# Performance work log

Measured on AMD Instinct MI355X. Metric: run time of the kernel, lower is better.

The kernel has to match this reference:

```python
import jax, jax.numpy as jnp
import numpy as np

B, N = 2, 6
FC, FH, FW = 256, 32, 88            # encoder feature shape
ORFH, ORFW = 256, 704               # original image H, W
OUT_C = 128
D_ST, D_END, D_STEP = 1.0, 60.0, 3.0
NXV, NYV, NZV = 256, 256, 1         # BEV voxel grid (x, y, z)
DXV = np.array([0.4, 0.4, 20.0], np.float32)          # dx
BXV = np.array([-51.0, -51.0, 0.0], np.float32)       # bx = bound_lo + dx/2
BN_EPS = 1e-3


def _conv(x, w, b):
    y = jax.lax.conv_general_dilated(x, w, (1, 1), 'SAME',
                                     dimension_numbers=('NCHW', 'OIHW', 'NCHW'))
    return y + b[None, :, None, None]


def _bn(x, scale, bias, mean, var):
    inv = scale / jnp.sqrt(var + BN_EPS)
    return x * inv[None, :, None, None] + (bias - mean * inv)[None, :, None, None]


def _frustum():
    ds = jnp.arange(D_ST, D_END, D_STEP, dtype=jnp.float32)      # (D,)
    xs = jnp.linspace(0.0, ORFW - 1.0, FW)
    ys = jnp.linspace(0.0, ORFH - 1.0, FH)
    f = jnp.stack(jnp.broadcast_arrays(xs[None, None, :], ys[None, :, None],
                                       ds[:, None, None]), axis=-1)  # (D,FH,FW,3)
    return f, ds


def _forward(cam2ego_rot, cam2ego_trans, cam_intrins, post_cam2ego_rot,
             post_cam2ego_trans, img_feats,
             conv1_w, conv1_b, bn1_s, bn1_b, bn1_m, bn1_v,
             conv2_w, conv2_b, bn2_s, bn2_b, bn2_m, bn2_v,
             conv3_w, conv3_b):
    frustum, depth_vals = _frustum()
    D = depth_vals.shape[0]
    # ---- geometry (GaussianLSS.get_geometry) ----
    pts = frustum[None, None] - post_cam2ego_trans[:, :, None, None, None, :]
    inv_post = jnp.linalg.inv(post_cam2ego_rot)                       # (B,N,3,3)
    pts = jnp.einsum('bnij,bndhwj->bndhwi', inv_post, pts)
    pts = jnp.concatenate([pts[..., :2] * pts[..., 2:3], pts[..., 2:3]], -1)
    combine = cam2ego_rot @ jnp.linalg.inv(cam_intrins)
    geometry = (jnp.einsum('bnij,bndhwj->bndhwi', combine, pts)
                + cam2ego_trans[:, :, None, None, None, :])           # (B,N,D,H,W,3)
    # ---- depth net + gaussian depth distribution (get_cam_feature) ----
    x = img_feats.reshape(B * N, FC, FH, FW)
    x = jax.nn.relu(_bn(_conv(x, conv1_w, conv1_b), bn1_s, bn1_b, bn1_m, bn1_v))
    x = jax.nn.relu(_bn(_conv(x, conv2_w, conv2_b), bn2_s, bn2_b, bn2_m, bn2_v))
    x = _conv(x, conv3_w, conv3_b)                                    # (BN, OUT_C+2, H, W)
    mu, log_sigma, feats = x[:, 0], x[:, 1], x[:, 2:]
    sigma = jnp.exp(log_sigma) + 1e-6
    g = jnp.exp(-0.5 * (depth_vals[None, :, None, None] - mu[:, None]) ** 2
                / (sigma[:, None] ** 2))                              # (BN,D,H,W)
    g = g / (jnp.sum(g, axis=1, keepdims=True) + 1e-6)
    vol = g[:, None] * feats[:, :, None]                              # (BN,C,D,H,W)
    vol = vol.reshape(B, N, OUT_C, D, FH, FW).transpose(0, 1, 3, 4, 5, 2)  # (B,N,D,H,W,C)
    # ---- bev_pool: voxelize + scatter-add ----
    dx = jnp.asarray(DXV)
    bx = jnp.asarray(BXV)
    geom = ((geometry - (bx - dx / 2.0)) / dx).astype(jnp.int32)      # trunc like .long()
    gx, gy, gz = geom[..., 0], geom[..., 1], geom[..., 2]
    kept = ((gx >= 0) & (gx < NXV) & (gy >= 0) & (gy < NYV)
            & (gz >= 0) & (gz < NZV))                                 # (B,N,D,H,W)
    bidx = jnp.arange(B, dtype=jnp.int32)[:, None, None, None, None]
    flat = ((bidx * NZV + gz) * NXV + gx) * NYV + gy
    flat = jnp.where(kept, flat, 0)
    w = kept.astype(vol.dtype)
    data = (vol * w[..., None]).reshape(-1, OUT_C)
    bev = jax.ops.segment_sum(data, flat.reshape(-1),
                              num_segments=B * NZV * NXV * NYV)
    # torch: (B,C,Z,X,Y) -> cat(unbind(dim=2), 1) -> (B, Z*C, X, Y)
    bev = bev.reshape(B, NZV, NXV, NYV, OUT_C).transpose(0, 1, 4, 2, 3)
    bev = bev.reshape(B, NZV * OUT_C, NXV, NYV)
    # ---- ref_bev_pool mask ----
    counts = jax.ops.segment_sum(w.reshape(-1), flat.reshape(-1),
                                 num_segments=B * NZV * NXV * NYV)
    mask = jnp.any(counts.reshape(B, NZV, NXV, NYV) > 0, axis=1)      # (B,X,Y) bool
    return bev, mask


def setup_inputs() -> dict:
    key = jax.random.key(0)
    ks = jax.random.split(key, 16)
    # camera->ego rotation: cam z -> ego x, cam x -> -ego y, cam y -> -ego z
    R = jnp.array([[0., 0., 1.], [-1., 0., 0.], [0., -1., 0.]], jnp.float32)
    cam2ego_rot = jnp.tile(R, (B, N, 1, 1)) + 0.01 * jax.random.normal(ks[0], (B, N, 3, 3))
    cam2ego_trans = jax.random.uniform(ks[1], (B, N, 3), minval=-2.0, maxval=2.0)
    K = jnp.array([[500., 0., ORFW / 2.], [0., 500., ORFH / 2.], [0., 0., 1.]], jnp.float32)
    cam_intrins = jnp.tile(K, (B, N, 1, 1))
    post_cam2ego_rot = jnp.tile(jnp.eye(3, dtype=jnp.float32), (B, N, 1, 1)) \
        + 0.005 * jax.random.normal(ks[2], (B, N, 3, 3))
    post_cam2ego_trans = 0.5 * jax.random.normal(ks[3], (B, N, 3))
    img_feats = 0.1 * jax.random.normal(ks[4], (B, N, FC, FH, FW))
    conv3_b = jnp.zeros((OUT_C + 2,)).at[0].set(25.0).at[1].set(2.3)  # mu~25m, sigma~10m
    return dict(
        cam2ego_rot=cam2ego_rot, cam2ego_trans=cam2ego_trans,
        cam_intrins=cam_intrins, post_cam2ego_rot=post_cam2ego_rot,
        post_cam2ego_trans=post_cam2ego_trans, img_feats=img_feats,
        conv1_w=0.02 * jax.random.normal(ks[5], (FC, FC, 3, 3)),
        conv1_b=jnp.zeros((FC,)),
        bn1_s=1.0 + 0.01 * jax.random.normal(ks[6], (FC,)),
        bn1_b=0.01 * jax.random.normal(ks[7], (FC,)),
        bn1_m=0.01 * jax.random.normal(ks[8], (FC,)),
        bn1_v=1.0 + 0.1 * jax.random.uniform(ks[9], (FC,)),
        conv2_w=0.02 * jax.random.normal(ks[10], (FC, FC, 3, 3)),
        conv2_b=jnp.zeros((FC,)),
        bn2_s=1.0 + 0.01 * jax.random.normal(ks[11], (FC,)),
        bn2_b=0.01 * jax.random.normal(ks[12], (FC,)),
        bn2_m=0.01 * jax.random.normal(ks[13], (FC,)),
        bn2_v=1.0 + 0.1 * jax.random.uniform(ks[14], (FC,)),
        conv3_w=0.02 * jax.random.normal(ks[15], (OUT_C + 2, FC, 1, 1)),
        conv3_b=conv3_b,
    )


def reference(cam2ego_rot, cam2ego_trans, cam_intrins, post_cam2ego_rot,
              post_cam2ego_trans, img_feats,
              conv1_w, conv1_b, bn1_s, bn1_b, bn1_m, bn1_v,
              conv2_w, conv2_b, bn2_s, bn2_b, bn2_m, bn2_v,
              conv3_w, conv3_b):
    return _forward(cam2ego_rot, cam2ego_trans, cam_intrins, post_cam2ego_rot,
                    post_cam2ego_trans, img_feats,
                    conv1_w, conv1_b, bn1_s, bn1_b, bn1_m, bn1_v,
                    conv2_w, conv2_b, bn2_s, bn2_b, bn2_m, bn2_v,
                    conv3_w, conv3_b)
```

## Files before the change

kernel.cpp:

```cpp
#include <hip/hip_runtime.h>
#include <math.h>

typedef unsigned short ushort_t;
typedef unsigned int uint_t;

#define NIMG 12
#define NCH  256
#define FH   32
#define FW   88
#define NPIX 2816
#define NDEP 20
#define NOUTC 128
#define NVOX 65536
#define NPTS 675840
#define NKEY 131072
#define NGP  33792
#define BEV_FLOATS 16777216u

#define B_OCC    0u
#define B_A1     4096u
#define B_C1     5120u
#define B_A2     6144u
#define B_C2     7168u
#define B_TOT    278528u
#define B_FEAT   282624u
#define B_VCODE  8933376u
#define B_WT     11636736u
#define B_CNT    14340096u
#define B_OFFS   14864384u
#define B_CUR    15388672u
#define B_SPINE  15912960u
#define B_RECS   17584128u
#define B_BEV    22990848u
#define B_XBF    29972480u
#define B_ACT1   47273984u
#define B_ACT2   64575488u
#define B_WSWZ1  81876992u
#define B_WSWZ2  83056640u
#define B_WSWZ3  84236288u

#define PREP_W2    2304
#define PREP_W3    4608
#define PREP_BN    4752
#define PREP_CAST0 4753
#define PREP_GEOM0 5281
#define PREP_NBLK  7921

#define GS_SCAN0   528
#define GS_NBLK    1040

#define SCAT_NBLK  2640
#define SCATZ_NBLK 4688

typedef __attribute__((ext_vector_type(8))) short bf16x8;
typedef __attribute__((ext_vector_type(4))) float floatx4;
typedef __attribute__((ext_vector_type(4))) uint_t u32x4;

__device__ __forceinline__ ushort_t f2bf(float f) {
    uint_t x = __float_as_uint(f);
    return (ushort_t)((x + 0x7fffu + ((x >> 16) & 1u)) >> 16);
}
__device__ __forceinline__ float bf2f(ushort_t u) {
    return __uint_as_float(((uint_t)u) << 16);
}

__device__ __forceinline__ void inv3x3(const float* __restrict__ M, float* __restrict__ o) {
    float a=M[0],b=M[1],c=M[2],d=M[3],e=M[4],f=M[5],g=M[6],h=M[7],i=M[8];
    float A = e*i - f*h;
    float B = c*h - b*i;
    float C = b*f - c*e;
    float D = f*g - d*i;
    float E = a*i - c*g;
    float F = c*d - a*f;
    float G = d*h - e*g;
    float H = b*g - a*h;
    float I = a*e - b*d;
    float det = a*A + b*D + c*G;
    float id = 1.0f / det;
    o[0]=A*id; o[1]=B*id; o[2]=C*id;
    o[3]=D*id; o[4]=E*id; o[5]=F*id;
    o[6]=G*id; o[7]=H*id; o[8]=I*id;
}

__device__ __forceinline__ void wprep_one(
    const float* __restrict__ w, ushort_t* __restrict__ dst,
    int ntap, int ncib, int ncog, int nco, int nci, int idx, bool split)
{
    int j = idx & 7;
    int l = (idx >> 3) & 63;
    int pairidx = idx >> 9;
    int g = pairidx % ncog;
    int b = (pairidx / ncog) % ncib;
    int t = pairidx / (ncog * ncib);
    int co = g * 16 + (l & 15);
    int ci = b * 32 + (l >> 4) * 8 + j;
    float v = 0.0f;
    if (co < nco) v = w[((size_t)co * nci + ci) * ntap + t];
    ushort_t hi = f2bf(v);
    if (split) {
        dst[(size_t)pairidx * 1024 + l * 8 + j]       = hi;
        dst[(size_t)pairidx * 1024 + 512 + l * 8 + j] = f2bf(v - bf2f(hi));
    } else {
        dst[(size_t)pairidx * 512 + l * 8 + j] = hi;
    }
}

__global__ __launch_bounds__(256) void prep_all_kernel(
    const float* __restrict__ w1, ushort_t* __restrict__ d1,
    const float* __restrict__ w2, ushort_t* __restrict__ d2,
    const float* __restrict__ w3, ushort_t* __restrict__ d3,
    const float* __restrict__ c2e_rot, const float* __restrict__ c2e_trans,
    const float* __restrict__ intrins, const float* __restrict__ post_rot,
    const float* __restrict__ post_trans,
    const float* __restrict__ c1b, const float* __restrict__ s1,
    const float* __restrict__ bb1, const float* __restrict__ m1, const float* __restrict__ v1,
    const float* __restrict__ c2b, const float* __restrict__ s2,
    const float* __restrict__ bb2, const float* __restrict__ m2, const float* __restrict__ v2,
    float* __restrict__ A1, float* __restrict__ C1,
    float* __restrict__ A2, float* __restrict__ C2,
    const float* __restrict__ img_in, ushort_t* __restrict__ xbf_out,
    int* __restrict__ vcode, uint_t* __restrict__ cnt)
{
    __shared__ __align__(16) ushort_t clds[64 * 264];
    int bid = blockIdx.x;
    int t = threadIdx.x;
    if (bid < PREP_W2) {
        wprep_one(w1, d1, 9, 8, 16, 256, 256, bid * 256 + t, false);
    } else if (bid < PREP_W3) {
        wprep_one(w2, d2, 9, 8, 16, 256, 256, (bid - PREP_W2) * 256 + t, false);
    } else if (bid < PREP_BN) {
        int idx = (bid - PREP_W3) * 256 + t;
        if (idx < 36864) wprep_one(w3, d3, 1, 8, 9, 130, 256, idx, true);
    } else if (bid == PREP_BN) {
        float i1 = s1[t] / sqrtf(v1[t] + 1e-3f);
        A1[t] = i1;
        C1[t] = (c1b[t] - m1[t]) * i1 + bb1[t];
        float i2 = s2[t] / sqrtf(v2[t] + 1e-3f);
        A2[t] = i2;
        C2[t] = (c2b[t] - m2[t]) * i2 + bb2[t];
    } else if (bid < PREP_GEOM0) {
        int cblk = bid - PREP_CAST0;
        int img = cblk / 44;
        int px0 = (cblk - img * 44) * 64;
        const float* src = img_in + (size_t)img * NCH * NPIX;
        int pxl = t & 63;
        int cib = t >> 6;
        #pragma unroll 4
        for (int cc = 0; cc < 64; ++cc) {
            int ci = cc * 4 + cib;
            float v = src[(size_t)ci * NPIX + px0 + pxl];
            clds[pxl * 264 + ci] = f2bf(v);
        }
        __syncthreads();
        int wv = t >> 6, lane = t & 63;
        uint2* outv = (uint2*)xbf_out;
        #pragma unroll
        for (int i = 0; i < 16; ++i) {
            int p = wv * 16 + i;
            uint2 val = *(const uint2*)&clds[p * 264 + lane * 4];
            outv[(size_t)(img * NPIX + px0 + p) * 64 + lane] = val;
        }
    } else {
        int i = (bid - PREP_GEOM0) * 256 + t;
        int lane = t & 63;
        int hw  = i % NPIX;
        int tmp = i / NPIX;
        int d   = tmp % NDEP;
        int bn  = tmp / NDEP;
        int h = hw / FW, w = hw - h * FW;
        float ip[9], ki[9], comb[9];
        inv3x3(post_rot + bn * 9, ip);
        inv3x3(intrins  + bn * 9, ki);
        const float* R = c2e_rot + bn * 9;
        #pragma unroll
        for (int r = 0; r < 3; ++r)
            #pragma unroll
            for (int cc = 0; cc < 3; ++cc)
                comb[r*3+cc] = R[r*3+0]*ki[0*3+cc] + R[r*3+1]*ki[1*3+cc] + R[r*3+2]*ki[2*3+cc];
        float xs = (float)w * (703.0f / 87.0f);
        float ys = (float)h * (255.0f / 31.0f);
        float dv = 1.0f + 3.0f * (float)d;
        float fx = xs - post_trans[bn*3+0];
        float fy = ys - post_trans[bn*3+1];
        float fz = dv - post_trans[bn*3+2];
        float p0 = ip[0]*fx + ip[1]*fy + ip[2]*fz;
        float p1 = ip[3]*fx + ip[4]*fy + ip[5]*fz;
        float p2 = ip[6]*fx + ip[7]*fy + ip[8]*fz;
        p0 *= p2; p1 *= p2;
        float gx = comb[0]*p0 + comb[1]*p1 + comb[2]*p2 + c2e_trans[bn*3+0];
        float gy = comb[3]*p0 + comb[4]*p1 + comb[5]*p2 + c2e_trans[bn*3+1];
        float gz = comb[6]*p0 + comb[7]*p1 + comb[8]*p2 + c2e_trans[bn*3+2];
        const float cx = -51.0f - 0.2f, cy = -51.0f - 0.2f, cz = 0.0f - 10.0f;
        int ix = (int)((gx - cx) / 0.4f);
        int iy = (int)((gy - cy) / 0.4f);
        int iz = (int)((gz - cz) / 20.0f);
        bool kept = (ix >= 0) && (ix < 256) && (iy >= 0) && (iy < 256) && (iz == 0);
        int code = kept ? ((ix << 8) | iy) : -1;
        vcode[i] = code;

        int b = bn / 6;
        uint_t key = kept ? (uint_t)((b << 16) | code) : 0xFFFFFFFFu;
        uint_t prevkey = __shfl_up(key, 1);
        bool leader = (lane == 0) || (key != prevkey);
        unsigned long long mask = __ballot(leader);
        if (leader && kept) {
            unsigned long long higher = mask & ~((2ULL << lane) - 1ULL);
            int nxt = higher ? (__ffsll((long long)higher) - 1) : 64;
            atomicAdd(&cnt[key], (uint_t)(nxt - lane));
        }
    }
}

__global__ __launch_bounds__(256, 3) void conv3x3_mfma(
    const ushort_t* __restrict__ in,
    const ushort_t* __restrict__ wswz,
    const float* __restrict__ Abn, const float* __restrict__ Cbn,
    ushort_t* __restrict__ out)
{
    __shared__ __align__(16) ushort_t lds[2][8640];
    int bx = blockIdx.x;
    int cg = blockIdx.y;
    int img = bx >> 5, h = bx & 31;
    int t = threadIdx.x;
    int w = t >> 6, l = t & 63;
    int q = l >> 4, c = l & 15;
    const int n0s[6] = {0, 16, 32, 48, 64, 72};

    for (int i = t; i < 8640; i += 256) ((uint_t*)lds)[i] = 0;

    const u32x4* src4 = (const u32x4*)(in + (size_t)img * NPIX * 256);
    const bf16x8* wsA = (const bf16x8*)wswz;

    int gbase[5], loff[5];
    bool sval[5];
    #pragma unroll
    for (int k = 0; k < 5; ++k) {
        int p = t + k * 256;
        bool valid = (p < 1056);
        int chunk = p >> 2, sub = p & 3;
        int r = chunk / 88;
        int col = chunk - r * 88;
        int hin = h - 1 + r;
        bool inb = valid && (hin >= 0) && (hin < FH);
        sval[k] = inb;
        gbase[k] = inb ? ((hin * 88 + col) * 32 + sub) : 0;
        int cs = col + 1;
        int slot = sub ^ ((cs >> 1) & 3);
        loff[k] = ((r * 90 + cs) * 4 + slot) * 8;
    }

    floatx4 acc[2][6];
    #pragma unroll
    for (int m = 0; m < 2; ++m)
        #pragma unroll
        for (int n = 0; n < 6; ++n)
            acc[m][n] = (floatx4){0.f, 0.f, 0.f, 0.f};

    int g0 = cg * 8 + w * 2;

    __syncthreads();
    #pragma unroll
    for (int k = 0; k < 5; ++k)
        if (sval[k]) *(u32x4*)&lds[0][loff[k]] = src4[gbase[k]];

    int buf = 0;
    for (int kb = 0; kb < 8; ++kb) {
        __syncthreads();
        u32x4 sreg[5];
        if (kb < 7) {
            #pragma unroll
            for (int k = 0; k < 5; ++k)
                if (sval[k]) sreg[k] = src4[gbase[k] + (kb + 1) * 4];
        }
        const bf16x8* B = (const bf16x8*)lds[buf];

        bf16x8 a0, a1;
        {
            int pa = (0 * 8 + kb) * 16;
            a0 = wsA[(size_t)(pa + g0    ) * 64 + l];
            a1 = wsA[(size_t)(pa + g0 + 1) * 64 + l];
        }
        #pragma unroll
        for (int t9 = 0; t9 < 9; ++t9) {
            bf16x8 na0, na1;
            if (t9 < 8) {
                int pa = ((t9 + 1) * 8 + kb) * 16;
                na0 = wsA[(size_t)(pa + g0    ) * 64 + l];
                na1 = wsA[(size_t)(pa + g0 + 1) * 64 + l];
            }
            int ky = t9 / 3, kx = t9 - ky * 3;
            #pragma unroll
            for (int n = 0; n < 6; ++n) {
                int col = n0s[n] + kx + c;
                int slot = q ^ ((col >> 1) & 3);
                bf16x8 b = B[(ky * 90 + col) * 4 + slot];
                acc[0][n] = __builtin_amdgcn_mfma_f32_16x16x32_bf16(a0, b, acc[0][n], 0, 0, 0);
                acc[1][n] = __builtin_amdgcn_mfma_f32_16x16x32_bf16(a1, b, acc[1][n], 0, 0, 0);
            }
            if (t9 < 8) { a0 = na0; a1 = na1; }
        }
        if (kb < 7) {
            #pragma unroll
            for (int k = 0; k < 5; ++k)
                if (sval[k]) *(u32x4*)&lds[buf ^ 1][loff[k]] = sreg[k];
        }
        buf ^= 1;
    }

    #pragma unroll
    for (int m = 0; m < 2; ++m) {
        int cob = cg * 128 + w * 32 + m * 16 + q * 4;
        float ba0 = Abn[cob+0], ba1 = Abn[cob+1], ba2 = Abn[cob+2], ba3 = Abn[cob+3];
        float bc0 = Cbn[cob+0], bc1 = Cbn[cob+1], bc2 = Cbn[cob+2], bc3 = Cbn[cob+3];
        #pragma unroll
        for (int n = 0; n < 6; ++n) {
            if (n == 5 && c < 8) continue;
            int col = n0s[n] + c;
            floatx4 v = acc[m][n];
            uint_t lo = (uint_t)f2bf(fmaxf(v[0]*ba0+bc0, 0.f)) | ((uint_t)f2bf(fmaxf(v[1]*ba1+bc1, 0.f)) << 16);
            uint_t hi = (uint_t)f2bf(fmaxf(v[2]*ba2+bc2, 0.f)) | ((uint_t)f2bf(fmaxf(v[3]*ba3+bc3, 0.f)) << 16);
            uint2 val; val.x = lo; val.y = hi;
            *(uint2*)&out[((size_t)img * NPIX + h * 88 + col) * 256 + cob] = val;
        }
    }
}

__global__ __launch_bounds__(256, 4) void gemm_scan_kernel(
    const ushort_t* __restrict__ act2,
    const ushort_t* __restrict__ wswz3,
    const float* __restrict__ b3,
    ushort_t* __restrict__ feat, float* __restrict__ wt,
    const uint_t* __restrict__ cnt, uint_t* __restrict__ offs,
    uint_t* __restrict__ spine)
{
    __shared__ uint_t s[256];
    int t = threadIdx.x;
    if (blockIdx.x >= GS_SCAN0) {
        int blk = blockIdx.x - GS_SCAN0;
        int i = blk * 256 + t;
        uint_t v = cnt[i];
        s[t] = v;
        __syncthreads();
        #pragma unroll
        for (int off = 1; off < 256; off <<= 1) {
            uint_t add = (t >= off) ? s[t - off] : 0u;
            __syncthreads();
            s[t] += add;
            __syncthreads();
        }
        offs[i] = s[t] - v;
        if (t == 255) spine[blk] = s[255];
        return;
    }
    int wv = t >> 6, l = t & 63, q = l >> 4, c = l & 15;
    int n0 = (blockIdx.x * 4 + wv) * 16;
    int px = n0 + c;
    const bf16x8* A = (const bf16x8*)wswz3;
    const bf16x8* B = (const bf16x8*)act2;
    floatx4 acc[9];
    #pragma unroll
    for (int g = 0; g < 9; ++g) acc[g] = (floatx4){0.f, 0.f, 0.f, 0.f};
    for (int kb = 0; kb < 8; ++kb) {
        bf16x8 b = B[(size_t)px * 32 + kb * 4 + q];
        #pragma unroll
        for (int g = 0; g < 9; ++g) {
            size_t pa = (size_t)(kb * 9 + g) * 128;
            acc[g] = __builtin_amdgcn_mfma_f32_16x16x32_bf16(A[pa + l],      b, acc[g], 0, 0, 0);
            acc[g] = __builtin_amdgcn_mfma_f32_16x16x32_bf16(A[pa + 64 + l], b, acc[g], 0, 0, 0);
        }
    }
    #pragma unroll
    for (int g = 0; g < 9; ++g) {
        #pragma unroll
        for (int r = 0; r < 4; ++r) {
            int co = g * 16 + q * 4 + r;
            if (co < 2 || co >= 130) continue;
            feat[(size_t)px * 128 + (co - 2)] = f2bf(acc[g][r] + b3[co]);
        }
    }
    float muv = acc[0][0] + b3[0];
    float lsv = acc[0][1] + b3[1];
    float mu_b  = __shfl(muv, c);
    float sig   = expf(__shfl(lsv, c)) + 1e-6f;
    float ninv2 = -0.5f / (sig * sig);
    float g5[5]; float sum = 0.0f;
    #pragma unroll
    for (int j = 0; j < 5; ++j) {
        float dv = 1.0f + 3.0f * (float)(q * 5 + j);
        float df = dv - mu_b;
        g5[j] = expf(df * df * ninv2);
        sum += g5[j];
    }
    sum += __shfl_xor(sum, 16);
    sum += __shfl_xor(sum, 32);
    float inv = 1.0f / (sum + 1e-6f);
    #pragma unroll
    for (int j = 0; j < 5; ++j)
        wt[(size_t)(q * 5 + j) * NGP + px] = g5[j] * inv;
}

__global__ __launch_bounds__(256) void fixup_kernel(
    uint_t* __restrict__ offs, const uint_t* __restrict__ spine,
    uint_t* __restrict__ cursor, const uint_t* __restrict__ cnt,
    float* __restrict__ mask_out, uint_t* __restrict__ total,
    unsigned char* __restrict__ occ)
{
    __shared__ uint_t red[256];
    int bid = blockIdx.x, t = threadIdx.x;
    uint_t part = 0;
    for (int j = t; j < bid; j += 256) part += spine[j];
    red[t] = part;
    __syncthreads();
    #pragma unroll
    for (int off = 128; off > 0; off >>= 1) {
        if (t < off) red[t] += red[t + off];
        __syncthreads();
    }
    uint_t prefix = red[0];
    int i = bid * 256 + t;
    uint_t o = offs[i] + prefix;
    offs[i] = o;
    cursor[i] = o;
    uint_t n = cnt[i];
    mask_out[i] = (n > 0) ? 1.0f : 0.0f;
    int lane = t & 63, wv = t >> 6;
    unsigned long long any = __ballot(n > 0u);
    if (lane == 0) occ[bid * 4 + wv] = any ? 1 : 0;
    if (i == NKEY - 1) *total = o + n;
}

__global__ __launch_bounds__(256) void scatter_zero_kernel(
    const int* __restrict__ vcode, const float* __restrict__ wt,
    uint_t* __restrict__ cursor, uint2* __restrict__ recs,
    const unsigned char* __restrict__ occ, float* __restrict__ bev_tmp)
{
    if (blockIdx.x >= SCAT_NBLK) {
        int blk = blockIdx.x - SCAT_NBLK;
        if (!occ[blk]) return;
        int b = blk >> 10;
        int v0 = (blk & 1023) * 64;
        floatx4* dst = (floatx4*)(bev_tmp + ((size_t)b * NVOX + v0) * NOUTC);
        int t = threadIdx.x;
        #pragma unroll
        for (int k = 0; k < 8; ++k)
            dst[k * 256 + t] = (floatx4){0.f, 0.f, 0.f, 0.f};
        return;
    }
    int i = blockIdx.x * 256 + threadIdx.x;
    int lane = threadIdx.x & 63;
    int code = vcode[i];
    int hw  = i % NPIX;
    int tmp = i / NPIX;
    int d   = tmp % NDEP;
    int bn  = tmp / NDEP;
    int b   = bn / 6;
    int gp  = bn * NPIX + hw;
    bool active = (code >= 0);
    uint_t key = active ? (uint_t)((b << 16) | code) : 0xFFFFFFFFu;
    uint2 r;
    r.x = ((uint_t)(code & 0xffff) << 16) | (uint_t)gp;
    r.y = active ? __float_as_uint(wt[(size_t)d * NGP + gp]) : 0u;

    uint_t prevkey = __shfl_up(key, 1);
    bool leader = (lane == 0) || (key != prevkey);
    unsigned long long mask = __ballot(leader);
    uint_t base = 0;
    if (leader && active) {
        unsigned long long higher = mask & ~((2ULL << lane) - 1ULL);
        int nxt = higher ? (__ffsll((long long)higher) - 1) : 64;
        base = atomicAdd(&cursor[key], (uint_t)(nxt - lane));
    }
    unsigned long long lower = mask & ((2ULL << lane) - 1ULL);
    int lead = 63 - __clzll((long long)lower);
    base = __shfl(base, lead);
    if (active) recs[base + (lane - lead)] = r;
}

__global__ __launch_bounds__(256) void segreduce_kernel(
    const uint2* __restrict__ recs, const uint_t* __restrict__ total,
    const uint_t* __restrict__ featu,
    float* __restrict__ bev_tmp)
{
    uint_t R = *total;
    int wid = blockIdx.x * 4 + (threadIdx.x >> 6);
    uint_t start = (uint_t)wid * 64u;
    if (start >= R) return;
    int lane = threadIdx.x & 63;
    uint_t ustart = __builtin_amdgcn_readfirstlane(start);

    uint_t myidx = ustart + (uint_t)lane;
    if (myidx >= R) myidx = R - 1u;
    uint2 mr = recs[myidx];

    uint_t rx0 = (uint_t)__shfl((int)mr.x, 0);
    uint_t gp00 = rx0 & 0xffffu;
    uint_t prevk = ((gp00 >= 16896u) ? 0x10000u : 0u) | (rx0 >> 16);
    float acc0 = 0.f, acc1 = 0.f;

    uint_t fbuf[2][16];
    #pragma unroll
    for (int j = 0; j < 16; ++j) {
        uint_t rx = (uint_t)__shfl((int)mr.x, j);
        fbuf[0][j] = featu[(size_t)(rx & 0xffffu) * 64 + lane];
    }
    #pragma unroll
    for (int b = 0; b < 4; ++b) {
        if (b < 3) {
            #pragma unroll
            for (int j = 0; j < 16; ++j) {
                uint_t rx = (uint_t)__shfl((int)mr.x, (b + 1) * 16 + j);
                fbuf[(b + 1) & 1][j] = featu[(size_t)(rx & 0xffffu) * 64 + lane];
            }
        }
        #pragma unroll
        for (int j = 0; j < 16; ++j) {
            int e = b * 16 + j;
            uint_t rx = (uint_t)__shfl((int)mr.x, e);
            uint_t ry = (uint_t)__shfl((int)mr.y, e);
            uint_t gp = rx & 0xffffu;
            uint_t key = ((gp >= 16896u) ? 0x10000u : 0u) | (rx >> 16);
            float wv = __uint_as_float(ry);
            if (ustart + (uint_t)e >= R) { key = prevk; wv = 0.f; }
            if (key != prevk) {
                float* p = bev_tmp + (size_t)prevk * NOUTC;
                atomicAdd(p + 2 * lane,     acc0);
                atomicAdd(p + 2 * lane + 1, acc1);
                acc0 = acc1 = 0.f;
                prevk = key;
            }
            uint_t fv = fbuf[b & 1][j];
            acc0 = fmaf(wv, bf2f((ushort_t)(fv & 0xffffu)), acc0);
            acc1 = fmaf(wv, bf2f((ushort_t)(fv >> 16)),     acc1);
        }
    }
    float* p = bev_tmp + (size_t)prevk * NOUTC;
    atomicAdd(p + 2 * lane,     acc0);
    atomicAdd(p + 2 * lane + 1, acc1);
}

__global__ __launch_bounds__(256) void transpose_kernel(
    const float* __restrict__ bev_tmp, const unsigned char* __restrict__ occ,
    float* __restrict__ bev_out)
{
    __shared__ float lds[64 * 129];
    int blk = blockIdx.x;
    int b   = blk >> 10;
    int v0  = (blk & 1023) * 64;
    int t   = threadIdx.x;
    float* dst = bev_out + (size_t)b * NOUTC * NVOX + v0;
    if (!occ[blk]) {
        #pragma unroll
        for (int k = 0; k < 32; ++k) {
            int idx = k * 256 + t;
            int vl = idx & 63, ch = idx >> 6;
            dst[(size_t)ch * NVOX + vl] = 0.0f;
        }
        return;
    }
    const float* src = bev_tmp + ((size_t)b * NVOX + v0) * NOUTC;
    #pragma unroll
    for (int k = 0; k < 32; ++k) {
        int idx = k * 256 + t;
        int v = idx >> 7, ch = idx & 127;
        lds[v * 129 + ch] = src[idx];
    }
    __syncthreads();
    #pragma unroll
    for (int k = 0; k < 32; ++k) {
        int idx = k * 256 + t;
        int vl = idx & 63, ch = idx >> 6;
        dst[(size_t)ch * NVOX + vl] = lds[vl * 129 + ch];
    }
}

extern "C" void kernel_launch(void* const* d_in, const int* in_sizes, int n_in,
                              void* d_out, int out_size, void* d_ws, size_t ws_size,
                              hipStream_t stream) {
    const float* c2e_rot    = (const float*)d_in[0];
    const float* c2e_trans  = (const float*)d_in[1];
    const float* intrins    = (const float*)d_in[2];
    const float* post_rot   = (const float*)d_in[3];
    const float* post_trans = (const float*)d_in[4];
    const float* img_feats  = (const float*)d_in[5];
    const float* conv1_w    = (const float*)d_in[6];
    const float* conv1_b    = (const float*)d_in[7];
    const float* bn1_s = (const float*)d_in[8];
    const float* bn1_b = (const float*)d_in[9];
    const float* bn1_m = (const float*)d_in[10];
    const float* bn1_v = (const float*)d_in[11];
    const float* conv2_w = (const float*)d_in[12];
    const float* conv2_b = (const float*)d_in[13];
    const float* bn2_s = (const float*)d_in[14];
    const float* bn2_b = (const float*)d_in[15];
    const float* bn2_m = (const float*)d_in[16];
    const float* bn2_v = (const float*)d_in[17];
    const float* conv3_w = (const float*)d_in[18];
    const float* conv3_b = (const float*)d_in[19];

    char* base = (char*)d_ws;
    unsigned char* occ = (unsigned char*)(base + B_OCC);
    float*    A1     = (float*)(base + B_A1);
    float*    C1     = (float*)(base + B_C1);
    float*    A2     = (float*)(base + B_A2);
    float*    C2     = (float*)(base + B_C2);
    uint_t*   total  = (uint_t*)(base + B_TOT);
    ushort_t* feat   = (ushort_t*)(base + B_FEAT);
    uint2*    recs   = (uint2*)(base + B_RECS);
    float*    bevtmp = (float*)(base + B_BEV);
    int*      vcode  = (int*)(base + B_VCODE);
    float*    wt     = (float*)(base + B_WT);
    uint_t*   cnt    = (uint_t*)(base + B_CNT);
    uint_t*   offs   = (uint_t*)(base + B_OFFS);
    uint_t*   cursor = (uint_t*)(base + B_CUR);
    uint_t*   spine  = (uint_t*)(base + B_SPINE);
    ushort_t* xbf    = (ushort_t*)(base + B_XBF);
    ushort_t* act1   = (ushort_t*)(base + B_ACT1);
    ushort_t* act2   = (ushort_t*)(base + B_ACT2);
    ushort_t* wswz1  = (ushort_t*)(base + B_WSWZ1);
    ushort_t* wswz2  = (ushort_t*)(base + B_WSWZ2);
    ushort_t* wswz3  = (ushort_t*)(base + B_WSWZ3);

    float* bev_out  = (float*)d_out;
    float* mask_out = bev_out + BEV_FLOATS;

    hipMemsetAsync(cnt, 0, NKEY * sizeof(uint_t), stream);
    prep_all_kernel<<<PREP_NBLK, 256, 0, stream>>>(
        conv1_w, wswz1, conv2_w, wswz2, conv3_w, wswz3,
        c2e_rot, c2e_trans, intrins, post_rot, post_trans,
        conv1_b, bn1_s, bn1_b, bn1_m, bn1_v,
        conv2_b, bn2_s, bn2_b, bn2_m, bn2_v,
        A1, C1, A2, C2,
        img_feats, xbf, vcode, cnt);
    conv3x3_mfma<<<dim3(NIMG * 32, 2), 256, 0, stream>>>(xbf,  wswz1, A1, C1, act1);
    conv3x3_mfma<<<dim3(NIMG * 32, 2), 256, 0, stream>>>(act1, wswz2, A2, C2, act2);
    gemm_scan_kernel<<<GS_NBLK, 256, 0, stream>>>(act2, wswz3, conv3_b, feat, wt,
                                                  cnt, offs, spine);
    fixup_kernel<<<NKEY / 256, 256, 0, stream>>>(offs, spine, cursor, cnt, mask_out, total, occ);
    scatter_zero_kernel<<<SCATZ_NBLK, 256, 0, stream>>>(vcode, wt, cursor, recs, occ, bevtmp);
    segreduce_kernel<<<(NPTS / 64 + 3) / 4, 256, 0, stream>>>(recs, total, (const uint_t*)feat, bevtmp);
    transpose_kernel<<<2048, 256, 0, stream>>>(bevtmp, occ, bev_out);
}
```

Measured before the change: 336.9 us.

## Compute all 256 output channels per conv block to halve input staging

The 3x3 conv kernel no longer splits output channels across two blocks. Each block now computes all 256 channels, with each wave handling four 16-channel M tiles instead of two. The input row tile is loaded into LDS once rather than twice, and each LDS B fragment feeds four MFMAs. In exchange the grid shrinks to 384 blocks, accumulator registers double, and launch bounds drop to 2 blocks per SM, which cuts occupancy and parallelism on a GPU with many CUs.

```diff
diff --git a/kernel.cpp b/kernel.cpp
--- a/kernel.cpp
+++ b/kernel.cpp
@@ -211,7 +211,7 @@
     }
 }
 
-__global__ __launch_bounds__(256, 3) void conv3x3_mfma(
+__global__ __launch_bounds__(256, 2) void conv3x3_mfma(
     const ushort_t* __restrict__ in,
     const ushort_t* __restrict__ wswz,
     const float* __restrict__ Abn, const float* __restrict__ Cbn,
@@ -219,7 +219,6 @@
 {
     __shared__ __align__(16) ushort_t lds[2][8640];
     int bx = blockIdx.x;
-    int cg = blockIdx.y;
     int img = bx >> 5, h = bx & 31;
     int t = threadIdx.x;
     int w = t >> 6, l = t & 63;
@@ -249,14 +248,14 @@
         loff[k] = ((r * 90 + cs) * 4 + slot) * 8;
     }
 
-    floatx4 acc[2][6];
-    #pragma unroll
-    for (int m = 0; m < 2; ++m)
+    floatx4 acc[4][6];
+    #pragma unroll
+    for (int m = 0; m < 4; ++m)
         #pragma unroll
         for (int n = 0; n < 6; ++n)
             acc[m][n] = (floatx4){0.f, 0.f, 0.f, 0.f};
 
-    int g0 = cg * 8 + w * 2;
+    int g0 = w * 4;
 
     __syncthreads();
     #pragma unroll
@@ -274,19 +273,21 @@
         }
         const bf16x8* B = (const bf16x8*)lds[buf];
 
-        bf16x8 a0, a1;
+        bf16x8 a[4];
         {
             int pa = (0 * 8 + kb) * 16;
-            a0 = wsA[(size_t)(pa + g0    ) * 64 + l];
-            a1 = wsA[(size_t)(pa + g0 + 1) * 64 + l];
+            #pragma unroll
+            for (int m = 0; m < 4; ++m)
+                a[m] = wsA[(size_t)(pa + g0 + m) * 64 + l];
         }
         #pragma unroll
         for (int t9 = 0; t9 < 9; ++t9) {
-            bf16x8 na0, na1;
+            bf16x8 na[4];
             if (t9 < 8) {
                 int pa = ((t9 + 1) * 8 + kb) * 16;
-                na0 = wsA[(size_t)(pa + g0    ) * 64 + l];
-                na1 = wsA[(size_t)(pa + g0 + 1) * 64 + l];
+                #pragma unroll
+                for (int m = 0; m < 4; ++m)
+                    na[m] = wsA[(size_t)(pa + g0 + m) * 64 + l];
             }
             int ky = t9 / 3, kx = t9 - ky * 3;
             #pragma unroll
@@ -294,10 +295,14 @@
                 int col = n0s[n] + kx + c;
                 int slot = q ^ ((col >> 1) & 3);
                 bf16x8 b = B[(ky * 90 + col) * 4 + slot];
-                acc[0][n] = __builtin_amdgcn_mfma_f32_16x16x32_bf16(a0, b, acc[0][n], 0, 0, 0);
-                acc[1][n] = __builtin_amdgcn_mfma_f32_16x16x32_bf16(a1, b, acc[1][n], 0, 0, 0);
+                #pragma unroll
+                for (int m = 0; m < 4; ++m)
+                    acc[m][n] = __builtin_amdgcn_mfma_f32_16x16x32_bf16(a[m], b, acc[m][n], 0, 0, 0);
             }
-            if (t9 < 8) { a0 = na0; a1 = na1; }
+            if (t9 < 8) {
+                #pragma unroll
+                for (int m = 0; m < 4; ++m) a[m] = na[m];
+            }
         }
         if (kb < 7) {
             #pragma unroll
@@ -308,8 +313,8 @@
     }
 
     #pragma unroll
-    for (int m = 0; m < 2; ++m) {
-        int cob = cg * 128 + w * 32 + m * 16 + q * 4;
+    for (int m = 0; m < 4; ++m) {
+        int cob = w * 64 + m * 16 + q * 4;
         float ba0 = Abn[cob+0], ba1 = Abn[cob+1], ba2 = Abn[cob+2], ba3 = Abn[cob+3];
         float bc0 = Cbn[cob+0], bc1 = Cbn[cob+1], bc2 = Cbn[cob+2], bc3 = Cbn[cob+3];
         #pragma unroll
@@ -631,8 +636,8 @@
         conv2_b, bn2_s, bn2_b, bn2_m, bn2_v,
         A1, C1, A2, C2,
         img_feats, xbf, vcode, cnt);
-    conv3x3_mfma<<<dim3(NIMG * 32, 2), 256, 0, stream>>>(xbf,  wswz1, A1, C1, act1);
-    conv3x3_mfma<<<dim3(NIMG * 32, 2), 256, 0, stream>>>(act1, wswz2, A2, C2, act2);
+    conv3x3_mfma<<<NIMG * 32, 256, 0, stream>>>(xbf,  wswz1, A1, C1, act1);
+    conv3x3_mfma<<<NIMG * 32, 256, 0, stream>>>(act1, wswz2, A2, C2, act2);
     gemm_scan_kernel<<<GS_NBLK, 256, 0, stream>>>(act2, wswz3, conv3_b, feat, wt,
                                                   cnt, offs, spine);
     fixup_kernel<<<NKEY / 256, 256, 0, stream>>>(offs, spine, cursor, cnt, mask_out, total, occ);
```

Result: no change. 333.8 us (-0.9%).
